# Performance work log

Hardware: AMD Instinct MI355X
Metric: run time of the kernel (lower is better)

Reference implementation:

```python
import jax, jax.numpy as jnp
import numpy as np

N, E, D = 100000, 600000, 128

def setup_inputs() -> dict:
    key = jax.random.key(0)
    ks = jax.random.split(key, 6)
    s = 1.0 / np.sqrt(D)
    return {
        "h": jax.random.normal(ks[0], (N, D), dtype=jnp.float32),
        "edge_index": jax.random.randint(ks[1], (2, E), 0, N, dtype=jnp.int64),
        "Wg": jax.random.normal(ks[2], (2 * D, D), dtype=jnp.float32) * s,
        "bg": jnp.zeros((D,), dtype=jnp.float32),
        "Ws": jax.random.normal(ks[3], (D, D), dtype=jnp.float32) * s,
        "bs": jnp.zeros((D,), dtype=jnp.float32),
        "Wr": jax.random.normal(ks[4], (D, D), dtype=jnp.float32) * s,
        "br": jnp.zeros((D,), dtype=jnp.float32),
    }

def reference(h, edge_index, Wg, bg, Ws, bs, Wr, br):
    send, rec = edge_index[0], edge_index[1]
    h_rec = h[rec]            # [E, D]
    h_send = h[send]          # [E, D]
    # gate: sigmoid(Linear(cat([h_rec, h_send])))  -- split W to avoid concat copy
    gate_in = h_rec @ Wg[:h.shape[1]] + h_send @ Wg[h.shape[1]:] + bg
    eta = jax.nn.sigmoid(gate_in)                      # [E, D]
    h_messages = eta * (h_send @ Ws + bs)              # [E, D]
    h_agg = jax.ops.segment_sum(h_messages, rec, num_segments=h.shape[0])
    return (h @ Wr + br) + h_agg
```

## Files before the change

kernel.cpp:

```cpp
#include <hip/hip_runtime.h>
#include <stdint.h>

#define FD 128

typedef __bf16 bf16x8 __attribute__((ext_vector_type(8)));
typedef unsigned short u16x8 __attribute__((ext_vector_type(8)));
typedef float  f32x16 __attribute__((ext_vector_type(16)));

__device__ __forceinline__ unsigned short f2bf(float f) {
    unsigned u = __float_as_uint(f);
    unsigned r = u + 0x7fffu + ((u >> 16) & 1u);
    return (unsigned short)(r >> 16);
}
__device__ __forceinline__ float bflo(unsigned u) { return __uint_as_float(u << 16); }
__device__ __forceinline__ float bfhi(unsigned u) { return __uint_as_float(u & 0xffff0000u); }


__global__ __launch_bounds__(256) void prep_kernel(
    const float* __restrict__ Wg,
    const float* __restrict__ Ws,
    const float* __restrict__ Wr,
    unsigned short* __restrict__ Wf,
    int* __restrict__ deg,
    int* __restrict__ partial,
    int N)
{
    int wid = blockIdx.x * 256 + threadIdx.x;
    for (int i = wid; i < N; i += 65536) deg[i] = 0;
    if (wid < 264) partial[wid] = 0;
    if (wid >= 512 * 128) return;
    int j  = wid & 7;
    int l  = (wid >> 3) & 63;
    int kt = (wid >> 9) & 7;
    int ct = wid >> 12;
    int k  = kt * 16 + (l >> 5) * 8 + j;
    int c  = ct * 32 + (l & 31);
    float v;
    if (c < 128)      v = Wg[k * FD + c];
    else if (c < 256) v = Wg[(128 + k) * FD + (c - 128)];
    else if (c < 384) v = Ws[k * FD + (c - 256)];
    else              v = Wr[k * FD + (c - 384)];
    Wf[wid] = f2bf(v);
}

__global__ __launch_bounds__(256, 4) void gemm_kernel(
    const float* __restrict__ h,
    const unsigned short* __restrict__ Wf,
    const float* __restrict__ bg,
    const float* __restrict__ bs,
    const float* __restrict__ br,
    unsigned short* __restrict__ A,
    unsigned short* __restrict__ BS,
    float* __restrict__ out,
    const int* __restrict__ idx,
    int* __restrict__ deg,
    int N, int E)
{
    __shared__ unsigned short Bsh[16384];

    if (blockIdx.y == 0) {
        int t = blockIdx.x * 256 + threadIdx.x;
        for (int e = t; e < E; e += 65536) atomicAdd(&deg[idx[E + e]], 1);
        return;
    }

    const int w    = blockIdx.y - 1;
    const int lane = threadIdx.x & 63;
    const int wid  = threadIdx.x >> 6;

    {
        const unsigned short* src = Wf + (size_t)w * 16384 + (size_t)threadIdx.x * 8;
        unsigned short* dst = Bsh + (size_t)threadIdx.x * 8;
        #pragma unroll
        for (int p = 0; p < 8; ++p) {
            __builtin_amdgcn_global_load_lds(
                (const __attribute__((address_space(1))) void*)(src + p * 2048),
                (__attribute__((address_space(3))) void*)(dst + p * 2048),
                16, 0, 0);
        }
    }

    const int col_l  = lane & 31;
    const int rhalf  = (lane >> 5) * 4;
    float bias[4];
    #pragma unroll
    for (int i = 0; i < 4; ++i) {
        int col = i * 32 + col_l;
        bias[i] = (w == 0) ? bg[col] : (w == 2) ? bs[col] : (w == 3) ? br[col] : 0.0f;
    }
    unsigned short* dst0 = (w == 0) ? A : (w == 2) ? (BS + 128) : BS;
    const size_t rstride = (w == 0) ? 128 : 256;

    __syncthreads();

    const int stride = gridDim.x * 128;
    for (int rb0 = blockIdx.x * 128; rb0 < N; rb0 += stride) {
        const int rb = rb0 + wid * 32;
        int arow = rb + (lane & 31);
        if (arow >= N) arow = N - 1;
        const float* aptr = h + (size_t)arow * FD + (lane >> 5) * 8;

        bf16x8 afrag[8];
        #pragma unroll
        for (int kt = 0; kt < 8; ++kt) {
            float4 f0 = *(const float4*)(aptr + kt * 16);
            float4 f1 = *(const float4*)(aptr + kt * 16 + 4);
            union { u16x8 u; bf16x8 b; } cv;
            cv.u[0] = f2bf(f0.x); cv.u[1] = f2bf(f0.y);
            cv.u[2] = f2bf(f0.z); cv.u[3] = f2bf(f0.w);
            cv.u[4] = f2bf(f1.x); cv.u[5] = f2bf(f1.y);
            cv.u[6] = f2bf(f1.z); cv.u[7] = f2bf(f1.w);
            afrag[kt] = cv.b;
        }

        f32x16 acc[4];
        #pragma unroll
        for (int i = 0; i < 4; ++i)
            #pragma unroll
            for (int r = 0; r < 16; ++r) acc[i][r] = 0.0f;

        #pragma unroll
        for (int kt = 0; kt < 8; ++kt) {
            #pragma unroll
            for (int i = 0; i < 4; ++i) {
                bf16x8 bfr = *(const bf16x8*)(Bsh + (size_t)((i * 8 + kt) * 64 + lane) * 8);
                acc[i] = __builtin_amdgcn_mfma_f32_32x32x16_bf16(
                             afrag[kt], bfr, acc[i], 0, 0, 0);
            }
        }

        const bool interior = (rb + 32 <= N);
        if (w == 3) {
            #pragma unroll
            for (int i = 0; i < 4; ++i) {
                int col = i * 32 + col_l;
                #pragma unroll
                for (int r = 0; r < 16; ++r) {
                    int row = rb + (r & 3) + 8 * (r >> 2) + rhalf;
                    if (interior || row < N)
                        out[(size_t)row * FD + col] = acc[i][r] + bias[i];
                }
            }
        } else {
            #pragma unroll
            for (int i = 0; i < 4; ++i) {
                int col = i * 32 + col_l;
                #pragma unroll
                for (int r = 0; r < 16; ++r) {
                    int row = rb + (r & 3) + 8 * (r >> 2) + rhalf;
                    if (interior || row < N)
                        dst0[(size_t)row * rstride + col] = f2bf(acc[i][r] + bias[i]);
                }
            }
        }
    }
}

__global__ __launch_bounds__(256) void scan_kernel(
    int* __restrict__ deg, unsigned* __restrict__ partial, int N)
{
    __shared__ int sh[256];
    __shared__ int sh2[256];
    const int bid = blockIdx.x;
    const int tid = threadIdx.x;
    int base = bid * 1024 + tid * 4;
    int v[4];
    #pragma unroll
    for (int j = 0; j < 4; ++j) v[j] = (base + j < N) ? deg[base + j] : 0;
    int tsum = v[0] + v[1] + v[2] + v[3];
    sh[tid] = tsum;
    __syncthreads();
    for (int ofs = 1; ofs < 256; ofs <<= 1) {
        int x = (tid >= ofs) ? sh[tid - ofs] : 0;
        __syncthreads();
        sh[tid] += x;
        __syncthreads();
    }
    if (tid == 0) atomicExch(&partial[bid], 0x80000000u | (unsigned)sh[255]);
    int myagg = 0;
    if (tid < bid) {
        unsigned p;
        do { p = atomicAdd(&partial[tid], 0u); } while (!(p & 0x80000000u));
        myagg = (int)(p & 0x7fffffffu);
    }
    sh2[tid] = myagg;
    __syncthreads();
    for (int ofs = 128; ofs > 0; ofs >>= 1) {
        if (tid < ofs) sh2[tid] += sh2[tid + ofs];
        __syncthreads();
    }
    int run = sh2[0] + sh[tid] - tsum;
    #pragma unroll
    for (int j = 0; j < 4; ++j) {
        if (base + j < N) deg[base + j] = run;
        run += v[j];
    }
}

__global__ __launch_bounds__(256) void scatter_kernel(
    const int* __restrict__ idx, int* __restrict__ off,
    int* __restrict__ csr, int E)
{
    int e = blockIdx.x * 256 + threadIdx.x;
    if (e >= E) return;
    int s = idx[e];
    int r = idx[E + e];
    int pos = atomicAdd(&off[r], 1);
    csr[pos] = s;
}

__global__ __launch_bounds__(256) void aggregate_kernel(
    const int* __restrict__ off,
    const int* __restrict__ csr,
    const unsigned* __restrict__ A,
    const unsigned* __restrict__ BS,
    float* __restrict__ out,
    int N)
{
    int r = blockIdx.x * 4 + (threadIdx.x >> 6);
    if (r >= N) return;
    int lane = threadIdx.x & 63;

    int start = (r == 0) ? 0 : off[r - 1];
    int end   = off[r];
    if (start >= end) return;

    unsigned ua = A[(size_t)r * 64 + lane];
    float a0 = bflo(ua), a1 = bfhi(ua);
    float acc0 = 0.0f, acc1 = 0.0f;

    int i = start;
    for (; i + 3 < end; i += 4) {
        int s0 = csr[i], s1 = csr[i + 1], s2 = csr[i + 2], s3 = csr[i + 3];
        unsigned ub0 = BS[(size_t)s0 * 128 + lane];
        unsigned us0 = BS[(size_t)s0 * 128 + 64 + lane];
        unsigned ub1 = BS[(size_t)s1 * 128 + lane];
        unsigned us1 = BS[(size_t)s1 * 128 + 64 + lane];
        unsigned ub2 = BS[(size_t)s2 * 128 + lane];
        unsigned us2 = BS[(size_t)s2 * 128 + 64 + lane];
        unsigned ub3 = BS[(size_t)s3 * 128 + lane];
        unsigned us3 = BS[(size_t)s3 * 128 + 64 + lane];
        acc0 += bflo(us0) * __builtin_amdgcn_rcpf(1.0f + __expf(-(a0 + bflo(ub0))));
        acc1 += bfhi(us0) * __builtin_amdgcn_rcpf(1.0f + __expf(-(a1 + bfhi(ub0))));
        acc0 += bflo(us1) * __builtin_amdgcn_rcpf(1.0f + __expf(-(a0 + bflo(ub1))));
        acc1 += bfhi(us1) * __builtin_amdgcn_rcpf(1.0f + __expf(-(a1 + bfhi(ub1))));
        acc0 += bflo(us2) * __builtin_amdgcn_rcpf(1.0f + __expf(-(a0 + bflo(ub2))));
        acc1 += bfhi(us2) * __builtin_amdgcn_rcpf(1.0f + __expf(-(a1 + bfhi(ub2))));
        acc0 += bflo(us3) * __builtin_amdgcn_rcpf(1.0f + __expf(-(a0 + bflo(ub3))));
        acc1 += bfhi(us3) * __builtin_amdgcn_rcpf(1.0f + __expf(-(a1 + bfhi(ub3))));
    }
    for (; i < end; ++i) {
        int s0 = csr[i];
        unsigned ub0 = BS[(size_t)s0 * 128 + lane];
        unsigned us0 = BS[(size_t)s0 * 128 + 64 + lane];
        acc0 += bflo(us0) * __builtin_amdgcn_rcpf(1.0f + __expf(-(a0 + bflo(ub0))));
        acc1 += bfhi(us0) * __builtin_amdgcn_rcpf(1.0f + __expf(-(a1 + bfhi(ub0))));
    }

    float2* o = (float2*)(out + (size_t)r * FD + 2 * lane);
    float2 cur = *o;
    cur.x += acc0;
    cur.y += acc1;
    *o = cur;
}

extern "C" void kernel_launch(void* const* d_in, const int* in_sizes, int n_in,
                              void* d_out, int out_size, void* d_ws, size_t ws_size,
                              hipStream_t stream)
{
    const float* h  = (const float*)d_in[0];
    const int*   ei = (const int*)d_in[1];
    const float* Wg = (const float*)d_in[2];
    const float* bg = (const float*)d_in[3];
    const float* Ws = (const float*)d_in[4];
    const float* bs = (const float*)d_in[5];
    const float* Wr = (const float*)d_in[6];
    const float* br = (const float*)d_in[7];
    float* out = (float*)d_out;

    const int N = in_sizes[0] / FD;
    const int E = in_sizes[1] / 2;

    unsigned short* Wf  = (unsigned short*)d_ws;
    unsigned short* Abf = Wf + 512 * FD;
    unsigned short* BSb = Abf + (size_t)N * FD;
    int* deg     = (int*)(BSb + (size_t)N * 2 * FD);
    int* partial = deg + N;
    int* csr     = partial + 264;

    size_t need = (size_t)(512 * FD + 3ull * N * FD) * 2 + ((size_t)N + 264 + E) * 4;
    if (ws_size < need) return;

    const int nb = (N + 1023) / 1024;
    if (nb > 256) return;

    prep_kernel<<<256, 256, 0, stream>>>(Wg, Ws, Wr, Wf, deg, partial, N);
    dim3 ggrid(256, 5);
    gemm_kernel<<<ggrid, 256, 0, stream>>>(h, Wf, bg, bs, br,
                                           Abf, BSb, out, ei, deg, N, E);
    scan_kernel<<<nb, 256, 0, stream>>>(deg, (unsigned*)partial, N);
    scatter_kernel<<<(E + 255) / 256, 256, 0, stream>>>(ei, deg, csr, E);
    aggregate_kernel<<<(N + 3) / 4, 256, 0, stream>>>(deg, csr,
                                                      (const unsigned*)Abf,
                                                      (const unsigned*)BSb,
                                                      out, N);
}
```

Before: 272.0 us.

## Fuse degree scan into GEMM kernel and stage bf16 stores through LDS

The separate scan kernel is folded into the GEMM launch as an extra grid row. Those blocks spin on a global counter until all degree-counting blocks finish, then run the decoupled prefix scan, which removes one kernel launch and lets the scan overlap the GEMM. The bf16 output epilogue now stages each 4-row slice in shared memory and writes 16-byte coalesced rows instead of scattered 2-byte stores. In exchange it adds block barriers per slice, relies on spin-waits that could deadlock if the counting blocks cannot be scheduled, and the counter at partial[260] must be reset by prep_kernel.

Result: slower. 296.4 us (+9.0%).

```diff
diff --git a/kernel.cpp b/kernel.cpp
--- a/kernel.cpp
+++ b/kernel.cpp
@@ -54,13 +54,67 @@
     float* __restrict__ out,
     const int* __restrict__ idx,
     int* __restrict__ deg,
+    int* __restrict__ partial,
     int N, int E)
 {
     __shared__ unsigned short Bsh[16384];
+    __shared__ uint4 EshQ[256];
 
     if (blockIdx.y == 0) {
         int t = blockIdx.x * 256 + threadIdx.x;
         for (int e = t; e < E; e += 65536) atomicAdd(&deg[idx[E + e]], 1);
+        __syncthreads();
+        __threadfence();
+        if (threadIdx.x == 0) atomicAdd(&partial[260], 1);
+        return;
+    }
+
+    if (blockIdx.y == 5) {
+        const int nb = (N + 1023) >> 10;
+        if (blockIdx.x >= nb) return;
+        if (threadIdx.x == 0) {
+            while (atomicAdd(&partial[260], 0) < 256) __builtin_amdgcn_s_sleep(8);
+        }
+        __syncthreads();
+        int* sh  = (int*)Bsh;
+        int* sh2 = sh + 256;
+        const int bid = blockIdx.x;
+        const int tid = threadIdx.x;
+        int base = bid * 1024 + tid * 4;
+        int v[4];
+        #pragma unroll
+        for (int j = 0; j < 4; ++j)
+            v[j] = (base + j < N) ? atomicAdd(&deg[base + j], 0) : 0;
+        int tsum = v[0] + v[1] + v[2] + v[3];
+        sh[tid] = tsum;
+        __syncthreads();
+        for (int ofs = 1; ofs < 256; ofs <<= 1) {
+            int x = (tid >= ofs) ? sh[tid - ofs] : 0;
+            __syncthreads();
+            sh[tid] += x;
+            __syncthreads();
+        }
+        if (tid == 0)
+            atomicExch((unsigned*)&partial[bid], 0x80000000u | (unsigned)sh[255]);
+        int myagg = 0;
+        if (tid < bid) {
+            unsigned p;
+            do { p = atomicAdd((unsigned*)&partial[tid], 0u); }
+            while (!(p & 0x80000000u));
+            myagg = (int)(p & 0x7fffffffu);
+        }
+        sh2[tid] = myagg;
+        __syncthreads();
+        for (int ofs = 128; ofs > 0; ofs >>= 1) {
+            if (tid < ofs) sh2[tid] += sh2[tid + ofs];
+            __syncthreads();
+        }
+        int run = sh2[0] + sh[tid] - tsum;
+        #pragma unroll
+        for (int j = 0; j < 4; ++j) {
+            if (base + j < N) deg[base + j] = run;
+            run += v[j];
+        }
         return;
     }
 
@@ -90,6 +144,7 @@
     }
     unsigned short* dst0 = (w == 0) ? A : (w == 2) ? (BS + 128) : BS;
     const size_t rstride = (w == 0) ? 128 : 256;
+    unsigned short* eb = (unsigned short*)(EshQ + (size_t)wid * 64);
 
     __syncthreads();
 
@@ -143,57 +198,44 @@
             }
         } else {
             #pragma unroll
-            for (int i = 0; i < 4; ++i) {
-                int col = i * 32 + col_l;
-                #pragma unroll
-                for (int r = 0; r < 16; ++r) {
-                    int row = rb + (r & 3) + 8 * (r >> 2) + rhalf;
-                    if (interior || row < N)
-                        dst0[(size_t)row * rstride + col] = f2bf(acc[i][r] + bias[i]);
+            for (int q = 0; q < 8; ++q) {
+                const int b = q >> 1;
+                const bool mine = ((lane >> 5) == (q & 1));
+                if (interior) {
+                    if (mine) {
+                        #pragma unroll
+                        for (int j = 0; j < 4; ++j) {
+                            #pragma unroll
+                            for (int i = 0; i < 4; ++i)
+                                eb[j * 128 + i * 32 + col_l] =
+                                    f2bf(acc[i][4 * b + j] + bias[i]);
+                        }
+                    }
+                } else {
+                    if (mine) {
+                        #pragma unroll
+                        for (int j = 0; j < 4; ++j) {
+                            int row = rb + 4 * q + j;
+                            if (row < N) {
+                                #pragma unroll
+                                for (int i = 0; i < 4; ++i)
+                                    dst0[(size_t)row * rstride + i * 32 + col_l] =
+                                        f2bf(acc[i][4 * b + j] + bias[i]);
+                            }
+                        }
+                    }
                 }
+                __syncthreads();
+                if (interior) {
+                    int lr = lane >> 4;
+                    int c  = lane & 15;
+                    uint4 vq = *(const uint4*)((const char*)eb + lane * 16);
+                    int grow = rb + 4 * q + lr;
+                    *(uint4*)(dst0 + (size_t)grow * rstride + c * 8) = vq;
+                }
+                __syncthreads();
             }
         }
-    }
-}
-
-__global__ __launch_bounds__(256) void scan_kernel(
-    int* __restrict__ deg, unsigned* __restrict__ partial, int N)
-{
-    __shared__ int sh[256];
-    __shared__ int sh2[256];
-    const int bid = blockIdx.x;
-    const int tid = threadIdx.x;
-    int base = bid * 1024 + tid * 4;
-    int v[4];
-    #pragma unroll
-    for (int j = 0; j < 4; ++j) v[j] = (base + j < N) ? deg[base + j] : 0;
-    int tsum = v[0] + v[1] + v[2] + v[3];
-    sh[tid] = tsum;
-    __syncthreads();
-    for (int ofs = 1; ofs < 256; ofs <<= 1) {
-        int x = (tid >= ofs) ? sh[tid - ofs] : 0;
-        __syncthreads();
-        sh[tid] += x;
-        __syncthreads();
-    }
-    if (tid == 0) atomicExch(&partial[bid], 0x80000000u | (unsigned)sh[255]);
-    int myagg = 0;
-    if (tid < bid) {
-        unsigned p;
-        do { p = atomicAdd(&partial[tid], 0u); } while (!(p & 0x80000000u));
-        myagg = (int)(p & 0x7fffffffu);
-    }
-    sh2[tid] = myagg;
-    __syncthreads();
-    for (int ofs = 128; ofs > 0; ofs >>= 1) {
-        if (tid < ofs) sh2[tid] += sh2[tid + ofs];
-        __syncthreads();
-    }
-    int run = sh2[0] + sh[tid] - tsum;
-    #pragma unroll
-    for (int j = 0; j < 4; ++j) {
-        if (base + j < N) deg[base + j] = run;
-        run += v[j];
     }
 }
 
@@ -295,10 +337,10 @@
     if (nb > 256) return;
 
     prep_kernel<<<256, 256, 0, stream>>>(Wg, Ws, Wr, Wf, deg, partial, N);
-    dim3 ggrid(256, 5);
+    dim3 ggrid(256, 6);
     gemm_kernel<<<ggrid, 256, 0, stream>>>(h, Wf, bg, bs, br,
-                                           Abf, BSb, out, ei, deg, N, E);
-    scan_kernel<<<nb, 256, 0, stream>>>(deg, (unsigned*)partial, N);
+                                           Abf, BSb, out, ei, deg, partial,
+                                           N, E);
     scatter_kernel<<<(E + 255) / 256, 256, 0, stream>>>(ei, deg, csr, E);
     aggregate_kernel<<<(N + 3) / 4, 256, 0, stream>>>(deg, csr,
                                                       (const unsigned*)Abf,
```
